# Kernel optimization log

Measured on AMD Instinct MI355X. Metric: run time of the kernel, lower is better.

Reference implementation:

```python
import jax, jax.numpy as jnp
import numpy as np
import math

N_HEAD = 32
ROPE_BASE = 10000.0


def _rope_headwise(x):
    # Faithful to the source bug: x is [B, H, S, D] and the rotary module uses
    # x.shape[1] (= H) as the "sequence length", so the angle depends on the
    # head index, broadcast over the true sequence axis.
    B, H, S, D = x.shape
    inv_freq = 1.0 / (ROPE_BASE ** (jnp.arange(0, D, 2, dtype=jnp.float32) / D))  # [D/2]
    t = jnp.arange(H, dtype=jnp.float32)                                          # [H]
    freqs = t[:, None] * inv_freq[None, :]                                        # [H, D/2]
    # emb = cat(freqs, freqs)[..., :D//2] == freqs, so cos/sin are just over freqs
    cos = jnp.cos(freqs)[None, :, None, :]   # [1, H, 1, D/2]
    sin = jnp.sin(freqs)[None, :, None, :]
    x1, x2 = x[..., : D // 2], x[..., D // 2 :]
    return jnp.concatenate([x1 * cos - x2 * sin, x1 * sin + x2 * cos], axis=-1)


def setup_inputs() -> dict:
    key = jax.random.key(0)
    ks = jax.random.split(key, 5)
    B, S, E = 2, 2048, 2048
    scale = 0.02
    return {
        "x": jax.random.normal(ks[0], (B, S, E), dtype=jnp.float32),
        "Wq": jax.random.normal(ks[1], (E, E), dtype=jnp.float32) * scale,
        "bq": jnp.zeros((E,), dtype=jnp.float32),
        "Wk": jax.random.normal(ks[2], (E, E), dtype=jnp.float32) * scale,
        "bk": jnp.zeros((E,), dtype=jnp.float32),
        "Wv": jax.random.normal(ks[3], (E, E), dtype=jnp.float32) * scale,
        "bv": jnp.zeros((E,), dtype=jnp.float32),
        "Wo": jax.random.normal(ks[4], (E, E), dtype=jnp.float32) * scale,
        "bo": jnp.zeros((E,), dtype=jnp.float32),
    }


def reference(x, Wq, bq, Wk, bk, Wv, bv, Wo, bo):
    B, S, E = x.shape
    H = N_HEAD
    D = E // H

    def split_heads(y):  # [B,S,E] -> [B,H,S,D]
        return y.reshape(B, S, H, D).transpose(0, 2, 1, 3)

    q = split_heads(x @ Wq + bq)
    k = split_heads(x @ Wk + bk)
    v = split_heads(x @ Wv + bv)

    q = _rope_headwise(q)
    k = _rope_headwise(k)

    scores = jnp.einsum("bhqd,bhkd->bhqk", q, k) / math.sqrt(D)  # [B,H,S,S]
    causal = jnp.triu(jnp.ones((S, S), dtype=bool), k=1)
    scores = jnp.where(causal[None, None], -jnp.inf, scores)
    attn = jax.nn.softmax(scores, axis=-1)
    out = jnp.einsum("bhqk,bhkd->bhqd", attn, v)                 # [B,H,S,D]
    out = out.transpose(0, 2, 1, 3).reshape(B, S, E)
    return out @ Wo + bo
```

## Files before the change

### kernel.cpp

```cpp
#include <hip/hip_runtime.h>
#include <hip/hip_bf16.h>

#define B_ 2
#define S_ 2048
#define E_ 2048
#define H_ 32
#define M_ (B_*S_)

typedef __bf16 bf16x8 __attribute__((ext_vector_type(8)));
typedef float  f32x4  __attribute__((ext_vector_type(4)));

__device__ __forceinline__ ushort f2bf(float f) {
    uint u = __float_as_uint(f);
    u += 0x7fffu + ((u >> 16) & 1u);
    return (ushort)(u >> 16);
}
__device__ __forceinline__ uint pack2bf(float a, float b) {
    __hip_bfloat162 h = __float22bfloat162_rn(make_float2(a, b));
    return *(uint*)&h;
}
__device__ __forceinline__ float fexp2(float x) {
#if __has_builtin(__builtin_amdgcn_exp2f)
    return __builtin_amdgcn_exp2f(x);
#else
    return exp2f(x);
#endif
}
__device__ __forceinline__ f32x4 f4zero() {
    f32x4 z; z[0]=0.f; z[1]=0.f; z[2]=0.f; z[3]=0.f; return z;
}
__device__ __forceinline__ void async16(const ushort* g, ushort* l) {
    __builtin_amdgcn_global_load_lds((const __attribute__((address_space(1))) void*)g,
                                     (__attribute__((address_space(3))) void*)l, 16, 0, 0);
}

__global__ __launch_bounds__(256) void cast_x_kernel(const float* __restrict__ x,
                                                     ushort* __restrict__ xb) {
    int i = (blockIdx.x * 256 + threadIdx.x) * 4;
    float4 v = *(const float4*)(x + i);
    uint2 o;
    o.x = pack2bf(v.x, v.y);
    o.y = pack2bf(v.z, v.w);
    *(uint2*)(xb + i) = o;
}

__global__ __launch_bounds__(256) void wtrans_kernel(const float* __restrict__ W0, const float* __restrict__ W1,
                                                     const float* __restrict__ W2, const float* __restrict__ W3,
                                                     ushort* __restrict__ T0, ushort* __restrict__ T1,
                                                     ushort* __restrict__ T2, ushort* __restrict__ T3) {
    const float* W = (blockIdx.z==0)?W0:(blockIdx.z==1)?W1:(blockIdx.z==2)?W2:W3;
    ushort*      T = (blockIdx.z==0)?T0:(blockIdx.z==1)?T1:(blockIdx.z==2)?T2:T3;
    __shared__ float tile[64][65];
    const int k0 = blockIdx.y * 64, n0 = blockIdx.x * 64;
    const int rr = threadIdx.x >> 4;
    const int cc = (threadIdx.x & 15) * 4;
    #pragma unroll
    for (int p = 0; p < 4; ++p) {
        int r = p * 16 + rr;
        float4 v = *(const float4*)(W + (size_t)(k0 + r) * E_ + n0 + cc);
        tile[r][cc+0] = v.x; tile[r][cc+1] = v.y; tile[r][cc+2] = v.z; tile[r][cc+3] = v.w;
    }
    __syncthreads();
    #pragma unroll
    for (int p = 0; p < 4; ++p) {
        int rn = p * 16 + rr;
        uint2 o;
        o.x = pack2bf(tile[cc+0][rn], tile[cc+1][rn]);
        o.y = pack2bf(tile[cc+2][rn], tile[cc+3][rn]);
        *(uint2*)(T + (size_t)(n0 + rn) * E_ + k0 + cc) = o;
    }
}

__global__ __launch_bounds__(256) void vtrans_kernel(const ushort* __restrict__ vb,
                                                     ushort* __restrict__ vt) {
    __shared__ ushort tile[64][65];
    const int bh = blockIdx.y, b = bh >> 5, h = bh & 31;
    const int s0 = blockIdx.x * 64;
    int tx = threadIdx.x & 63, ty = threadIdx.x >> 6;
    #pragma unroll
    for (int it = 0; it < 16; ++it) {
        int r = it * 4 + ty;
        tile[r][tx] = vb[(size_t)(b * S_ + s0 + r) * E_ + h * 64 + tx];
    }
    __syncthreads();
    #pragma unroll
    for (int it = 0; it < 16; ++it) {
        int r = it * 4 + ty;
        vt[(size_t)(bh * 64 + r) * S_ + s0 + tx] = tile[tx][r];
    }
}

#define VMW4 asm volatile("s_waitcnt vmcnt(4)" ::: "memory")
#define VMW0 asm volatile("s_waitcnt vmcnt(0)" ::: "memory")
#define MEMB asm volatile("" ::: "memory")

#define STA_(bf, kt, h) { _Pragma("unroll") for (int it_ = 0; it_ < 2; ++it_) { \
    async16(A + (size_t)(m0 + it_*128 + (h)*64 + srow) * E_ + (kt)*64 + scg*8,  \
            &As[bf][(it_*128 + (h)*64 + wave*8) * 64]); } }

#define STB_(bf, kt, h) { _Pragma("unroll") for (int it_ = 0; it_ < 2; ++it_) { \
    int rih_ = it_*64 + srow;                                                   \
    int ldr_ = ((rih_ >> 5) << 6) + (h)*32 + (rih_ & 31);                       \
    int rwb_ = it_*64 + wave*8;                                                 \
    int wbs_ = ((rwb_ >> 5) << 6) + (h)*32 + (rwb_ & 31);                       \
    async16(Bt + (size_t)(n0 + ldr_) * E_ + (kt)*64 + scg*8,                    \
            &Bs[bf][wbs_ * 64]); } }

#define PHASE_(bf, mh, nh, LA, LB, STAGES) {                                    \
    if (LA) {                                                                   \
      _Pragma("unroll") for (int m_ = 0; m_ < 4; ++m_)                          \
        _Pragma("unroll") for (int k_ = 0; k_ < 2; ++k_) {                      \
          int row_ = wm*128 + ((mh)*4 + m_)*16 + l15;                           \
          pa[m_][k_] = *(const bf16x8*)(&As[bf][row_*64 + (((k_*4 + quad) ^ (row_ & 7)) << 3)]); } } \
    if (LB) {                                                                   \
      _Pragma("unroll") for (int n_ = 0; n_ < 2; ++n_)                          \
        _Pragma("unroll") for (int k_ = 0; k_ < 2; ++k_) {                      \
          int row_ = wn*64 + ((nh)*2 + n_)*16 + l15;                            \
          pb[n_][k_] = *(const bf16x8*)(&Bs[bf][row_*64 + (((k_*4 + quad) ^ (row_ & 7)) << 3)]); } } \
    STAGES;                                                                     \
    MEMB; __builtin_amdgcn_s_barrier();                                         \
    __builtin_amdgcn_s_setprio(1);                                              \
    _Pragma("unroll") for (int k_ = 0; k_ < 2; ++k_)                            \
      _Pragma("unroll") for (int m_ = 0; m_ < 4; ++m_)                          \
        _Pragma("unroll") for (int n_ = 0; n_ < 2; ++n_)                        \
          acc[(mh)*4+m_][(nh)*2+n_] = __builtin_amdgcn_mfma_f32_16x16x32_bf16(  \
              pa[m_][k_], pb[n_][k_], acc[(mh)*4+m_][(nh)*2+n_], 0, 0, 0);      \
    __builtin_amdgcn_s_setprio(0);                                              \
    asm volatile("s_waitcnt lgkmcnt(0)" ::: "memory");                          \
    __builtin_amdgcn_sched_barrier(0);                                          \
    MEMB; __builtin_amdgcn_s_barrier(); MEMB;                                   \
  }

template<bool OUTF32, bool DOROPE, int NZ>
__global__ __launch_bounds__(512, 2) void gemm256(const ushort* __restrict__ A,
        const ushort* __restrict__ Bt0, const ushort* __restrict__ Bt1, const ushort* __restrict__ Bt2,
        const float* __restrict__ bias0, const float* __restrict__ bias1, const float* __restrict__ bias2,
        void* __restrict__ C0, void* __restrict__ C1, void* __restrict__ C2) {
    const int bid = blockIdx.x;
    const int z   = bid % NZ;
    const int nb  = (bid / NZ) % (E_ / 256);
    const int mb  = bid / (NZ * (E_ / 256));

    const ushort* Bt  = (z==0)?Bt0:(z==1)?Bt1:Bt2;
    const float* bias = (z==0)?bias0:(z==1)?bias1:bias2;
    void* Cv          = (z==0)?C0:(z==1)?C1:C2;

    __shared__ ushort As[2][256 * 64];
    __shared__ ushort Bs[2][256 * 64];

    const int tid  = threadIdx.x;
    const int wave = tid >> 6, lane = tid & 63;
    const int quad = lane >> 4, l15 = lane & 15;
    const int wm = wave >> 2, wn = wave & 3;
    const int m0 = mb * 256, n0 = nb * 256;
    const int srow = tid >> 3;
    const int scg  = (tid & 7) ^ (srow & 7);

    f32x4 acc[8][4];
    #pragma unroll
    for (int i = 0; i < 8; ++i)
        #pragma unroll
        for (int j = 0; j < 4; ++j) acc[i][j] = f4zero();

    bf16x8 pa[4][2], pb[2][2];

    STA_(0, 0, 0); STA_(0, 0, 1); STB_(0, 0, 0); STB_(0, 0, 1);
    STA_(1, 1, 0); STB_(1, 1, 0);
    VMW4;
    MEMB; __builtin_amdgcn_s_barrier(); MEMB;

    #pragma unroll 1
    for (int i = 0; i < 15; ++i) {
        const int t1 = 2*i + 1, t2 = 2*i + 2, t3 = 2*i + 3;
        PHASE_(0, 0, 1, 1, 1, STB_(1, t1, 1));
        PHASE_(0, 0, 0, 0, 1, STA_(1, t1, 1));
        PHASE_(0, 1, 0, 1, 0, STA_(0, t2, 0));
        PHASE_(0, 1, 1, 0, 1, STB_(0, t2, 0); VMW4);
        PHASE_(1, 0, 1, 1, 1, STB_(0, t2, 1));
        PHASE_(1, 0, 0, 0, 1, STA_(0, t2, 1));
        PHASE_(1, 1, 0, 1, 0, STA_(1, t3, 0));
        PHASE_(1, 1, 1, 0, 1, STB_(1, t3, 0); VMW4);
    }
    PHASE_(0, 0, 1, 1, 1, STB_(1, 31, 1));
    PHASE_(0, 0, 0, 0, 1, STA_(1, 31, 1));
    PHASE_(0, 1, 0, 1, 0, {});
    PHASE_(0, 1, 1, 0, 1, VMW0);
    PHASE_(1, 0, 1, 1, 1, {});
    PHASE_(1, 0, 0, 0, 1, {});
    PHASE_(1, 1, 0, 1, 0, {});
    PHASE_(1, 1, 1, 0, 1, {});

    if (DOROPE && z != 2) {
        const float qsc = (z == 0) ? 0.125f * 1.44269504f : 1.0f;
        const int h = (n0 + wn * 64) >> 6;
        float sn[2], cs[2];
        #pragma unroll
        for (int nt = 0; nt < 2; ++nt) {
            int j = nt * 16 + l15;
            float ang = (float)h * __expf(-(float)j * 0.28782313662425575f);
            __sincosf(ang, &sn[nt], &cs[nt]);
        }
        ushort* C = (ushort*)Cv;
        #pragma unroll
        for (int f = 0; f < 8; ++f) {
            #pragma unroll
            for (int nt = 0; nt < 2; ++nt) {
                int col1 = n0 + wn * 64 + nt * 16 + l15;
                float b1 = bias[col1], b2 = bias[col1 + 32];
                #pragma unroll
                for (int r = 0; r < 4; ++r) {
                    int rowg = m0 + wm * 128 + f * 16 + quad * 4 + r;
                    float x1 = acc[f][nt][r] + b1;
                    float x2 = acc[f][nt + 2][r] + b2;
                    C[(size_t)rowg * E_ + col1]      = f2bf((x1 * cs[nt] - x2 * sn[nt]) * qsc);
                    C[(size_t)rowg * E_ + col1 + 32] = f2bf((x1 * sn[nt] + x2 * cs[nt]) * qsc);
                }
            }
        }
    } else {
        #pragma unroll
        for (int f = 0; f < 8; ++f) {
            #pragma unroll
            for (int nt = 0; nt < 4; ++nt) {
                int col = n0 + wn * 64 + nt * 16 + l15;
                float bv = bias[col];
                #pragma unroll
                for (int r = 0; r < 4; ++r) {
                    int rowg = m0 + wm * 128 + f * 16 + quad * 4 + r;
                    float v = acc[f][nt][r] + bv;
                    if (OUTF32) ((float*)Cv)[(size_t)rowg * E_ + col] = v;
                    else        ((ushort*)Cv)[(size_t)rowg * E_ + col] = f2bf(v);
                }
            }
        }
    }
}
#undef STA_
#undef STB_
#undef PHASE_

template<bool OUTF32, bool DOROPE, int NZ>
__global__ __launch_bounds__(256) void gemm128(const ushort* __restrict__ A,
        const ushort* __restrict__ Bt0, const ushort* __restrict__ Bt1, const ushort* __restrict__ Bt2,
        const float* __restrict__ bias0, const float* __restrict__ bias1, const float* __restrict__ bias2,
        void* __restrict__ C0, void* __restrict__ C1, void* __restrict__ C2) {
    const int bid = blockIdx.x;
    const int z   = bid % NZ;
    const int nb  = (bid / NZ) % (E_ / 128);
    const int mb  = bid / (NZ * (E_ / 128));

    const ushort* Bt  = (z==0)?Bt0:(z==1)?Bt1:Bt2;
    const float* bias = (z==0)?bias0:(z==1)?bias1:bias2;
    void* Cv          = (z==0)?C0:(z==1)?C1:C2;

    __shared__ ushort As[128 * 64];
    __shared__ ushort Bs[128 * 64];

    const int tid  = threadIdx.x;
    const int wave = tid >> 6, lane = tid & 63;
    const int quad = lane >> 4, l15 = lane & 15;
    const int wm = wave >> 1, wn = wave & 1;
    const int m0 = mb * 128, n0 = nb * 128;
    const int srow = tid >> 3;
    const int scgx = (tid & 7) ^ (srow & 7);

    f32x4 acc[4][4];
    #pragma unroll
    for (int i = 0; i < 4; ++i)
        #pragma unroll
        for (int j = 0; j < 4; ++j) acc[i][j] = f4zero();

    for (int k0 = 0; k0 < E_; k0 += 64) {
        #pragma unroll
        for (int it = 0; it < 4; ++it) {
            int r = it * 32 + srow;
            async16(A  + (size_t)(m0 + r) * E_ + k0 + scgx * 8, As + (it * 256 + wave * 64) * 8);
            async16(Bt + (size_t)(n0 + r) * E_ + k0 + scgx * 8, Bs + (it * 256 + wave * 64) * 8);
        }
        __syncthreads();
        #pragma unroll
        for (int kk = 0; kk < 2; ++kk) {
            bf16x8 af[4], bfr[4];
            #pragma unroll
            for (int mt = 0; mt < 4; ++mt) {
                int row = wm * 64 + mt * 16 + l15;
                af[mt] = *(const bf16x8*)(As + row * 64 + (((kk * 4 + quad) ^ (row & 7)) << 3));
            }
            #pragma unroll
            for (int nt = 0; nt < 4; ++nt) {
                int row = wn * 64 + nt * 16 + l15;
                bfr[nt] = *(const bf16x8*)(Bs + row * 64 + (((kk * 4 + quad) ^ (row & 7)) << 3));
            }
            #pragma unroll
            for (int mt = 0; mt < 4; ++mt)
                #pragma unroll
                for (int nt = 0; nt < 4; ++nt)
                    acc[mt][nt] = __builtin_amdgcn_mfma_f32_16x16x32_bf16(af[mt], bfr[nt], acc[mt][nt], 0, 0, 0);
        }
        __syncthreads();
    }

    if (DOROPE && z != 2) {
        const float qsc = (z == 0) ? 0.125f * 1.44269504f : 1.0f;
        const int h = (n0 + wn * 64) >> 6;
        float sn[2], cs[2];
        #pragma unroll
        for (int nt = 0; nt < 2; ++nt) {
            int j = nt * 16 + l15;
            float ang = (float)h * __expf(-(float)j * 0.28782313662425575f);
            __sincosf(ang, &sn[nt], &cs[nt]);
        }
        ushort* C = (ushort*)Cv;
        #pragma unroll
        for (int mt = 0; mt < 4; ++mt) {
            #pragma unroll
            for (int nt = 0; nt < 2; ++nt) {
                int col1 = n0 + wn * 64 + nt * 16 + l15;
                float b1 = bias[col1], b2 = bias[col1 + 32];
                #pragma unroll
                for (int r = 0; r < 4; ++r) {
                    int rowg = m0 + wm * 64 + mt * 16 + quad * 4 + r;
                    float x1 = acc[mt][nt][r] + b1;
                    float x2 = acc[mt][nt + 2][r] + b2;
                    C[(size_t)rowg * E_ + col1]      = f2bf((x1 * cs[nt] - x2 * sn[nt]) * qsc);
                    C[(size_t)rowg * E_ + col1 + 32] = f2bf((x1 * sn[nt] + x2 * cs[nt]) * qsc);
                }
            }
        }
    } else {
        #pragma unroll
        for (int mt = 0; mt < 4; ++mt) {
            #pragma unroll
            for (int nt = 0; nt < 4; ++nt) {
                int col = n0 + wn * 64 + nt * 16 + l15;
                float bv = bias[col];
                #pragma unroll
                for (int r = 0; r < 4; ++r) {
                    int rowg = m0 + wm * 64 + mt * 16 + quad * 4 + r;
                    float v = acc[mt][nt][r] + bv;
                    if (OUTF32) ((float*)Cv)[(size_t)rowg * E_ + col] = v;
                    else        ((ushort*)Cv)[(size_t)rowg * E_ + col] = f2bf(v);
                }
            }
        }
    }
}

__global__ __launch_bounds__(512) void flash_kernel(const ushort* __restrict__ qb,
        const ushort* __restrict__ kb, const ushort* __restrict__ vt,
        ushort* __restrict__ ctx) {
    __shared__ ushort KVs[2][2][64 * 64];
    __shared__ ushort Ps[8][16 * 64];

    const int tid  = threadIdx.x;
    const int wave = tid >> 6, lane = tid & 63;
    const int quad = lane >> 4, l15 = lane & 15;
    const int bh = blockIdx.y, b = bh >> 5, h = bh & 31;
    const int srow = tid >> 3;
    const int scgx = (tid & 7) ^ (srow & 7);
    ushort* Pw = Ps[wave];

    bf16x8 ones;
    #pragma unroll
    for (int j = 0; j < 8; ++j) ones[j] = (__bf16)1.0f;

    #pragma unroll 1
    for (int pass = 0; pass < 2; ++pass) {
        const int qx  = pass ? (15 - (int)blockIdx.x) : (int)blockIdx.x;
        const int q0  = qx * 128;
        const int qw0 = q0 + wave * 16;
        const int nkt = 2 * qx + 2;

        bf16x8 qf[2];
        #pragma unroll
        for (int kk = 0; kk < 2; ++kk)
            qf[kk] = *(const bf16x8*)(qb + (size_t)(b * S_ + qw0 + l15) * E_ + h * 64 + kk * 32 + quad * 8);

        f32x4 oacc[4], lacc = f4zero();
        #pragma unroll
        for (int dt = 0; dt < 4; ++dt) oacc[dt] = f4zero();

        async16(kb + (size_t)(b * S_ + srow) * E_ + h * 64 + scgx * 8, KVs[0][0] + wave * 512);
        async16(vt + (size_t)(bh * 64 + srow) * S_ + scgx * 8,         KVs[0][1] + wave * 512);
        __syncthreads();

        #pragma unroll 1
        for (int kt = 0; kt < nkt; ++kt) {
            const int k0 = kt * 64;
            if (kt + 1 < nkt) {
                const int kn = k0 + 64;
                async16(kb + (size_t)(b * S_ + kn + srow) * E_ + h * 64 + scgx * 8,
                        KVs[(kt + 1) & 1][0] + wave * 512);
                async16(vt + (size_t)(bh * 64 + srow) * S_ + kn + scgx * 8,
                        KVs[(kt + 1) & 1][1] + wave * 512);
            }

            if (k0 <= qw0 + 15) {
                const ushort* Ks = KVs[kt & 1][0];
                const ushort* Vs = KVs[kt & 1][1];
                f32x4 sacc[4];
                #pragma unroll
                for (int nt = 0; nt < 4; ++nt) sacc[nt] = f4zero();
                #pragma unroll
                for (int kk = 0; kk < 2; ++kk)
                    #pragma unroll
                    for (int nt = 0; nt < 4; ++nt) {
                        int row = nt * 16 + l15;
                        bf16x8 kf = *(const bf16x8*)(Ks + row * 64 + (((kk * 4 + quad) ^ (row & 7)) << 3));
                        sacc[nt] = __builtin_amdgcn_mfma_f32_16x16x32_bf16(kf, qf[kk], sacc[nt], 0, 0, 0);
                    }

                const bool dm = (k0 + 63 > qw0);
                const int swz = l15 & 7;
                if (dm) {
                    const int q = qw0 + l15;
                    #pragma unroll
                    for (int nt = 0; nt < 4; ++nt) {
                        float p[4];
                        #pragma unroll
                        for (int r = 0; r < 4; ++r) {
                            int s = k0 + nt * 16 + quad * 4 + r;
                            float e = fexp2(sacc[nt][r]);
                            p[r] = (s > q) ? 0.f : e;
                        }
                        uint2 pk;
                        pk.x = pack2bf(p[0], p[1]);
                        pk.y = pack2bf(p[2], p[3]);
                        *(uint2*)(Pw + l15 * 64 + (((nt * 2 + (quad >> 1)) ^ swz) << 3) + (quad & 1) * 4) = pk;
                    }
                } else {
                    #pragma unroll
                    for (int nt = 0; nt < 4; ++nt) {
                        uint2 pk;
                        pk.x = pack2bf(fexp2(sacc[nt][0]), fexp2(sacc[nt][1]));
                        pk.y = pack2bf(fexp2(sacc[nt][2]), fexp2(sacc[nt][3]));
                        *(uint2*)(Pw + l15 * 64 + (((nt * 2 + (quad >> 1)) ^ swz) << 3) + (quad & 1) * 4) = pk;
                    }
                }

                #pragma unroll
                for (int kk = 0; kk < 2; ++kk) {
                    bf16x8 pf = *(const bf16x8*)(Pw + l15 * 64 + (((kk * 4 + quad) ^ swz) << 3));
                    lacc = __builtin_amdgcn_mfma_f32_16x16x32_bf16(pf, ones, lacc, 0, 0, 0);
                    #pragma unroll
                    for (int dt = 0; dt < 4; ++dt) {
                        int row = dt * 16 + l15;
                        bf16x8 vf = *(const bf16x8*)(Vs + row * 64 + (((kk * 4 + quad) ^ (row & 7)) << 3));
                        oacc[dt] = __builtin_amdgcn_mfma_f32_16x16x32_bf16(pf, vf, oacc[dt], 0, 0, 0);
                    }
                }
            }
            __syncthreads();
        }

        #pragma unroll
        for (int r = 0; r < 4; ++r) {
            float inv = 1.0f / lacc[r];
            #pragma unroll
            for (int dt = 0; dt < 4; ++dt)
                ctx[(size_t)(b * S_ + qw0 + quad * 4 + r) * E_ + h * 64 + dt * 16 + l15] =
                    f2bf(oacc[dt][r] * inv);
        }
    }
}

extern "C" void kernel_launch(void* const* d_in, const int* in_sizes, int n_in,
                              void* d_out, int out_size, void* d_ws, size_t ws_size,
                              hipStream_t stream) {
    const float* x  = (const float*)d_in[0];
    const float* Wq = (const float*)d_in[1];
    const float* bq = (const float*)d_in[2];
    const float* Wk = (const float*)d_in[3];
    const float* bk = (const float*)d_in[4];
    const float* Wv = (const float*)d_in[5];
    const float* bv = (const float*)d_in[6];
    const float* Wo = (const float*)d_in[7];
    const float* bo = (const float*)d_in[8];
    float* out = (float*)d_out;

    ushort* p   = (ushort*)d_ws;
    ushort* xb  = p; p += (size_t)M_ * E_;
    ushort* wqt = p; p += (size_t)E_ * E_;
    ushort* wkt = p; p += (size_t)E_ * E_;
    ushort* wvt = p; p += (size_t)E_ * E_;
    ushort* wot = p; p += (size_t)E_ * E_;
    ushort* qb  = p; p += (size_t)M_ * E_;
    ushort* kb  = p; p += (size_t)M_ * E_;
    ushort* vb  = p; p += (size_t)M_ * E_;
    ushort* ctx = p; p += (size_t)M_ * E_;
    ushort* vt  = xb;

    cast_x_kernel<<<(M_ * E_) / 1024, 256, 0, stream>>>(x, xb);
    wtrans_kernel<<<dim3(E_ / 64, E_ / 64, 4), 256, 0, stream>>>(Wq, Wk, Wv, Wo, wqt, wkt, wvt, wot);
    gemm256<false, true, 2><<<(E_ / 256) * (M_ / 256) * 2, 512, 0, stream>>>(
        xb, wqt, wkt, wkt, bq, bk, bk, qb, kb, kb);
    gemm128<false, false, 1><<<(E_ / 128) * (M_ / 128), 256, 0, stream>>>(
        xb, wvt, wvt, wvt, bv, bv, bv, vb, vb, vb);
    vtrans_kernel<<<dim3(S_ / 64, B_ * H_), 256, 0, stream>>>(vb, vt);
    flash_kernel<<<dim3(8, B_ * H_), 512, 0, stream>>>(qb, kb, vt, ctx);
    gemm128<true, false, 1><<<(E_ / 128) * (M_ / 128), 256, 0, stream>>>(
        ctx, wot, wot, wot, bo, bo, bo, out, out, out);
}
```

Before: 364.9 us.

## Merge prep kernels, fuse V transpose into GEMM epilogue, widen gemm256 phases

Folds the x cast and weight transpose into a single prep kernel launch. The V projection GEMM now writes its output already transposed through an LDS staging buffer in the epilogue, so the separate vtrans kernel and its extra global round trip go away. The gemm256 main loop is regrouped from eight phases per iteration to four, each doing 4x4 MFMAs with more B fragments held in registers. This adds register pressure and changes the load/compute interleaving in the big GEMM.

Result: no change. 359.5 us (-1.5%).

```diff
diff --git a/kernel.cpp b/kernel.cpp
--- a/kernel.cpp
+++ b/kernel.cpp
@@ -34,24 +34,29 @@
                                      (__attribute__((address_space(3))) void*)l, 16, 0, 0);
 }
 
-__global__ __launch_bounds__(256) void cast_x_kernel(const float* __restrict__ x,
-                                                     ushort* __restrict__ xb) {
-    int i = (blockIdx.x * 256 + threadIdx.x) * 4;
-    float4 v = *(const float4*)(x + i);
-    uint2 o;
-    o.x = pack2bf(v.x, v.y);
-    o.y = pack2bf(v.z, v.w);
-    *(uint2*)(xb + i) = o;
-}
-
-__global__ __launch_bounds__(256) void wtrans_kernel(const float* __restrict__ W0, const float* __restrict__ W1,
-                                                     const float* __restrict__ W2, const float* __restrict__ W3,
-                                                     ushort* __restrict__ T0, ushort* __restrict__ T1,
-                                                     ushort* __restrict__ T2, ushort* __restrict__ T3) {
-    const float* W = (blockIdx.z==0)?W0:(blockIdx.z==1)?W1:(blockIdx.z==2)?W2:W3;
-    ushort*      T = (blockIdx.z==0)?T0:(blockIdx.z==1)?T1:(blockIdx.z==2)?T2:T3;
+#define NCAST ((M_*E_)/1024)
+__global__ __launch_bounds__(256) void prep_kernel(const float* __restrict__ x, ushort* __restrict__ xb,
+        const float* __restrict__ W0, const float* __restrict__ W1,
+        const float* __restrict__ W2, const float* __restrict__ W3,
+        ushort* __restrict__ T0, ushort* __restrict__ T1,
+        ushort* __restrict__ T2, ushort* __restrict__ T3) {
+    const int bid = blockIdx.x;
+    if (bid < NCAST) {
+        int i = (bid * 256 + threadIdx.x) * 4;
+        float4 v = *(const float4*)(x + i);
+        uint2 o;
+        o.x = pack2bf(v.x, v.y);
+        o.y = pack2bf(v.z, v.w);
+        *(uint2*)(xb + i) = o;
+        return;
+    }
+    const int wb = bid - NCAST;
+    const int z  = wb >> 10;
+    const int rem = wb & 1023;
+    const float* W = (z==0)?W0:(z==1)?W1:(z==2)?W2:W3;
+    ushort*      T = (z==0)?T0:(z==1)?T1:(z==2)?T2:T3;
     __shared__ float tile[64][65];
-    const int k0 = blockIdx.y * 64, n0 = blockIdx.x * 64;
+    const int k0 = (rem >> 5) * 64, n0 = (rem & 31) * 64;
     const int rr = threadIdx.x >> 4;
     const int cc = (threadIdx.x & 15) * 4;
     #pragma unroll
@@ -71,25 +76,6 @@
     }
 }
 
-__global__ __launch_bounds__(256) void vtrans_kernel(const ushort* __restrict__ vb,
-                                                     ushort* __restrict__ vt) {
-    __shared__ ushort tile[64][65];
-    const int bh = blockIdx.y, b = bh >> 5, h = bh & 31;
-    const int s0 = blockIdx.x * 64;
-    int tx = threadIdx.x & 63, ty = threadIdx.x >> 6;
-    #pragma unroll
-    for (int it = 0; it < 16; ++it) {
-        int r = it * 4 + ty;
-        tile[r][tx] = vb[(size_t)(b * S_ + s0 + r) * E_ + h * 64 + tx];
-    }
-    __syncthreads();
-    #pragma unroll
-    for (int it = 0; it < 16; ++it) {
-        int r = it * 4 + ty;
-        vt[(size_t)(bh * 64 + r) * S_ + s0 + tx] = tile[tx][r];
-    }
-}
-
 #define VMW4 asm volatile("s_waitcnt vmcnt(4)" ::: "memory")
 #define VMW0 asm volatile("s_waitcnt vmcnt(0)" ::: "memory")
 #define MEMB asm volatile("" ::: "memory")
@@ -106,25 +92,24 @@
     async16(Bt + (size_t)(n0 + ldr_) * E_ + (kt)*64 + scg*8,                    \
             &Bs[bf][wbs_ * 64]); } }
 
-#define PHASE_(bf, mh, nh, LA, LB, STAGES) {                                    \
-    if (LA) {                                                                   \
-      _Pragma("unroll") for (int m_ = 0; m_ < 4; ++m_)                          \
+#define PH4_(bf, mh, LB, STAGES) {                                              \
+    _Pragma("unroll") for (int m_ = 0; m_ < 4; ++m_)                            \
+      _Pragma("unroll") for (int k_ = 0; k_ < 2; ++k_) {                        \
+        int row_ = wm*128 + (mh)*64 + m_*16 + l15;                              \
+        pa[m_][k_] = *(const bf16x8*)(&As[bf][row_*64 + (((k_*4 + quad) ^ (row_ & 7)) << 3)]); } \
+    if (LB) {                                                                   \
+      _Pragma("unroll") for (int n_ = 0; n_ < 4; ++n_)                          \
         _Pragma("unroll") for (int k_ = 0; k_ < 2; ++k_) {                      \
-          int row_ = wm*128 + ((mh)*4 + m_)*16 + l15;                           \
-          pa[m_][k_] = *(const bf16x8*)(&As[bf][row_*64 + (((k_*4 + quad) ^ (row_ & 7)) << 3)]); } } \
-    if (LB) {                                                                   \
-      _Pragma("unroll") for (int n_ = 0; n_ < 2; ++n_)                          \
-        _Pragma("unroll") for (int k_ = 0; k_ < 2; ++k_) {                      \
-          int row_ = wn*64 + ((nh)*2 + n_)*16 + l15;                            \
+          int row_ = wn*64 + n_*16 + l15;                                       \
           pb[n_][k_] = *(const bf16x8*)(&Bs[bf][row_*64 + (((k_*4 + quad) ^ (row_ & 7)) << 3)]); } } \
     STAGES;                                                                     \
     MEMB; __builtin_amdgcn_s_barrier();                                         \
     __builtin_amdgcn_s_setprio(1);                                              \
     _Pragma("unroll") for (int k_ = 0; k_ < 2; ++k_)                            \
       _Pragma("unroll") for (int m_ = 0; m_ < 4; ++m_)                          \
-        _Pragma("unroll") for (int n_ = 0; n_ < 2; ++n_)                        \
-          acc[(mh)*4+m_][(nh)*2+n_] = __builtin_amdgcn_mfma_f32_16x16x32_bf16(  \
-              pa[m_][k_], pb[n_][k_], acc[(mh)*4+m_][(nh)*2+n_], 0, 0, 0);      \
+        _Pragma("unroll") for (int n_ = 0; n_ < 4; ++n_)                        \
+          acc[(mh)*4+m_][n_] = __builtin_amdgcn_mfma_f32_16x16x32_bf16(         \
+              pa[m_][k_], pb[n_][k_], acc[(mh)*4+m_][n_], 0, 0, 0);             \
     __builtin_amdgcn_s_setprio(0);                                              \
     asm volatile("s_waitcnt lgkmcnt(0)" ::: "memory");                          \
     __builtin_amdgcn_sched_barrier(0);                                          \
@@ -162,9 +147,10 @@
         #pragma unroll
         for (int j = 0; j < 4; ++j) acc[i][j] = f4zero();
 
-    bf16x8 pa[4][2], pb[2][2];
-
-    STA_(0, 0, 0); STA_(0, 0, 1); STB_(0, 0, 0); STB_(0, 0, 1);
+    bf16x8 pa[4][2];
+    bf16x8 pb[4][2];
+
+    STA_(0, 0, 0); STB_(0, 0, 0); STA_(0, 0, 1); STB_(0, 0, 1);
     STA_(1, 1, 0); STB_(1, 1, 0);
     VMW4;
     MEMB; __builtin_amdgcn_s_barrier(); MEMB;
@@ -172,23 +158,15 @@
     #pragma unroll 1
     for (int i = 0; i < 15; ++i) {
         const int t1 = 2*i + 1, t2 = 2*i + 2, t3 = 2*i + 3;
-        PHASE_(0, 0, 1, 1, 1, STB_(1, t1, 1));
-        PHASE_(0, 0, 0, 0, 1, STA_(1, t1, 1));
-        PHASE_(0, 1, 0, 1, 0, STA_(0, t2, 0));
-        PHASE_(0, 1, 1, 0, 1, STB_(0, t2, 0); VMW4);
-        PHASE_(1, 0, 1, 1, 1, STB_(0, t2, 1));
-        PHASE_(1, 0, 0, 0, 1, STA_(0, t2, 1));
-        PHASE_(1, 1, 0, 1, 0, STA_(1, t3, 0));
-        PHASE_(1, 1, 1, 0, 1, STB_(1, t3, 0); VMW4);
-    }
-    PHASE_(0, 0, 1, 1, 1, STB_(1, 31, 1));
-    PHASE_(0, 0, 0, 0, 1, STA_(1, 31, 1));
-    PHASE_(0, 1, 0, 1, 0, {});
-    PHASE_(0, 1, 1, 0, 1, VMW0);
-    PHASE_(1, 0, 1, 1, 1, {});
-    PHASE_(1, 0, 0, 0, 1, {});
-    PHASE_(1, 1, 0, 1, 0, {});
-    PHASE_(1, 1, 1, 0, 1, {});
+        PH4_(0, 0, 1, STB_(1, t1, 1); STA_(1, t1, 1));
+        PH4_(0, 1, 0, STA_(0, t2, 0); STB_(0, t2, 0); VMW4);
+        PH4_(1, 0, 1, STB_(0, t2, 1); STA_(0, t2, 1));
+        PH4_(1, 1, 0, STA_(1, t3, 0); STB_(1, t3, 0); VMW4);
+    }
+    PH4_(0, 0, 1, STB_(1, 31, 1); STA_(1, 31, 1));
+    PH4_(0, 1, 0, VMW0);
+    PH4_(1, 0, 1, {});
+    PH4_(1, 1, 0, {});
 
     if (DOROPE && z != 2) {
         const float qsc = (z == 0) ? 0.125f * 1.44269504f : 1.0f;
@@ -237,9 +215,9 @@
 }
 #undef STA_
 #undef STB_
-#undef PHASE_
-
-template<bool OUTF32, bool DOROPE, int NZ>
+#undef PH4_
+
+template<bool OUTF32, bool DOROPE, bool DOVT, int NZ>
 __global__ __launch_bounds__(256) void gemm128(const ushort* __restrict__ A,
         const ushort* __restrict__ Bt0, const ushort* __restrict__ Bt1, const ushort* __restrict__ Bt2,
         const float* __restrict__ bias0, const float* __restrict__ bias1, const float* __restrict__ bias2,
@@ -253,8 +231,9 @@
     const float* bias = (z==0)?bias0:(z==1)?bias1:bias2;
     void* Cv          = (z==0)?C0:(z==1)?C1:C2;
 
-    __shared__ ushort As[128 * 64];
-    __shared__ ushort Bs[128 * 64];
+    __shared__ ushort smem[2 * 128 * 64];
+    ushort* As = smem;
+    ushort* Bs = smem + 128 * 64;
 
     const int tid  = threadIdx.x;
     const int wave = tid >> 6, lane = tid & 63;
@@ -300,7 +279,40 @@
         __syncthreads();
     }
 
-    if (DOROPE && z != 2) {
+    if (DOVT) {
+        ushort* tbuf = smem;
+        ushort* VT = (ushort*)Cv;
+        const int b  = m0 >> 11;
+        const int s0 = m0 & (S_ - 1);
+        #pragma unroll 1
+        for (int p = 0; p < 2; ++p) {
+            if (wn == p) {
+                #pragma unroll
+                for (int mt = 0; mt < 4; ++mt)
+                    #pragma unroll
+                    for (int nt = 0; nt < 4; ++nt) {
+                        int cl = nt * 16 + l15;
+                        float bv = bias[n0 + p * 64 + cl];
+                        #pragma unroll
+                        for (int r = 0; r < 4; ++r) {
+                            int row = wm * 64 + mt * 16 + quad * 4 + r;
+                            tbuf[cl * 136 + row] = f2bf(acc[mt][nt][r] + bv);
+                        }
+                    }
+            }
+            __syncthreads();
+            {
+                int d = tid >> 2, ch = tid & 3;
+                int hh = (n0 + p * 64) >> 6;
+                const ushort* src = tbuf + d * 136 + ch * 32;
+                ushort* dst = VT + ((size_t)(b * H_ + hh) * 64 + d) * S_ + s0 + ch * 32;
+                #pragma unroll
+                for (int j = 0; j < 4; ++j)
+                    *(uint4*)(dst + j * 8) = *(const uint4*)(src + j * 8);
+            }
+            __syncthreads();
+        }
+    } else if (DOROPE && z != 2) {
         const float qsc = (z == 0) ? 0.125f * 1.44269504f : 1.0f;
         const int h = (n0 + wn * 64) >> 6;
         float sn[2], cs[2];
@@ -486,18 +498,15 @@
     ushort* wot = p; p += (size_t)E_ * E_;
     ushort* qb  = p; p += (size_t)M_ * E_;
     ushort* kb  = p; p += (size_t)M_ * E_;
-    ushort* vb  = p; p += (size_t)M_ * E_;
+    ushort* vt  = p; p += (size_t)M_ * E_;
     ushort* ctx = p; p += (size_t)M_ * E_;
-    ushort* vt  = xb;
-
-    cast_x_kernel<<<(M_ * E_) / 1024, 256, 0, stream>>>(x, xb);
-    wtrans_kernel<<<dim3(E_ / 64, E_ / 64, 4), 256, 0, stream>>>(Wq, Wk, Wv, Wo, wqt, wkt, wvt, wot);
+
+    prep_kernel<<<NCAST + 4096, 256, 0, stream>>>(x, xb, Wq, Wk, Wv, Wo, wqt, wkt, wvt, wot);
     gemm256<false, true, 2><<<(E_ / 256) * (M_ / 256) * 2, 512, 0, stream>>>(
         xb, wqt, wkt, wkt, bq, bk, bk, qb, kb, kb);
-    gemm128<false, false, 1><<<(E_ / 128) * (M_ / 128), 256, 0, stream>>>(
-        xb, wvt, wvt, wvt, bv, bv, bv, vb, vb, vb);
-    vtrans_kernel<<<dim3(S_ / 64, B_ * H_), 256, 0, stream>>>(vb, vt);
+    gemm128<false, false, true, 1><<<(E_ / 128) * (M_ / 128), 256, 0, stream>>>(
+        xb, wvt, wvt, wvt, bv, bv, bv, vt, vt, vt);
     flash_kernel<<<dim3(8, B_ * H_), 512, 0, stream>>>(qb, kb, vt, ctx);
-    gemm128<true, false, 1><<<(E_ / 128) * (M_ / 128), 256, 0, stream>>>(
+    gemm128<true, false, false, 1><<<(E_ / 128) * (M_ / 128), 256, 0, stream>>>(
         ctx, wot, wot, wot, bo, bo, bo, out, out, out);
 }
```
